# Kernel tuning notes

Hardware: AMD Instinct MI355X
Metric: run time of the kernel (lower is better)

## Reference

```python
import jax, jax.numpy as jnp
import numpy as np

B, H, W, D = 16, 14, 14, 512   # map_dim D == attention_dim A (required by broadcast add)
L, HID, A = 32, 512, 512


def setup_inputs() -> dict:
    key = jax.random.key(0)
    ks = jax.random.split(key, 8)
    s = 0.02
    return {
        "maps": jax.random.normal(ks[0], (B, H, W, D), jnp.float32),
        "hiddens": jax.random.normal(ks[1], (B, L, HID), jnp.float32),
        "W_hidden": jax.random.normal(ks[2], (A, HID), jnp.float32) * s,
        "b_hidden": jnp.zeros((A,), jnp.float32),
        "W_rect": jax.random.normal(ks[3], (1, A), jnp.float32) * s,
        "b_rect": jnp.zeros((1,), jnp.float32),
        "W_co": jax.random.normal(ks[4], (HID, D), jnp.float32) * s,
        "b_co": jnp.zeros((HID,), jnp.float32),
    }


def reference(maps, hiddens, W_hidden, b_hidden, W_rect, b_rect, W_co, b_co):
    b, h, w, d = maps.shape
    fmaps = maps.reshape(b, h * w, d)                       # (B, P, D)
    hlin = hiddens @ W_hidden.T + b_hidden                  # (B, L, A)
    # additive co-attention score: ReLU(fmaps + hlin) -> linear to scalar
    rect = jax.nn.relu(fmaps[:, None, :, :] + hlin[:, :, None, :])  # (B, L, P, A)
    scores = jnp.einsum('blpa,a->blp', rect, W_rect[0]) + b_rect[0]  # (B, L, P)
    attn = jax.nn.softmax(scores, axis=2)                   # softmax over pixels P
    ctx = jnp.einsum('blp,bpd->bld', attn, fmaps)           # (B, L, D)
    co_att = (ctx @ W_co.T + b_co) * hiddens                # (B, L, HID)
    return co_att, attn
```

## Files before the change

kernel.cpp:

```cpp
#include <hip/hip_runtime.h>
#include <math.h>


typedef __attribute__((ext_vector_type(8))) short short8;
typedef __attribute__((ext_vector_type(4))) float f32x4;

__device__ __forceinline__ unsigned f2bf_u(float x) {
    union { float f; unsigned u; } c; c.f = x;
    return (c.u + 0x7FFFu + ((c.u >> 16) & 1u)) >> 16;
}
__device__ __forceinline__ unsigned pack2(float lo, float hi) {
    return f2bf_u(lo) | (f2bf_u(hi) << 16);
}
__device__ __forceinline__ uint4 pack8(const float4 a, const float4 b) {
    uint4 r;
    r.x = pack2(a.x, a.y); r.y = pack2(a.z, a.w);
    r.z = pack2(b.x, b.y); r.w = pack2(b.z, b.w);
    return r;
}

template<int HMUL>
__global__ __launch_bounds__(256) void gemm_kernel(
    const float* __restrict__ Af, const float* __restrict__ Bf,
    const float* __restrict__ bias, const float* __restrict__ hmul,
    float* __restrict__ C)
{
    __shared__ __align__(16) char smem[65536];
    uint4* As = (uint4*)smem;
    uint4* Bs = (uint4*)(smem + 32768);
    float* red = (float*)smem;
    const int tid = threadIdx.x, bid = blockIdx.x;

    const int m0 = (bid >> 4) * 32, n0 = (bid & 15) * 32;
    #pragma unroll
    for (int j = 0; j < 8; ++j) {
        const int S = tid + 256 * j;
        const int i = S >> 6, ln = S & 63;
        const int t = i & 1, s = i >> 1;
        const int row  = t * 16 + (ln & 15);
        const int col8 = s * 4 + (ln >> 4);
        const float* ap = Af + (size_t)(m0 + row) * 512 + col8 * 8;
        const float* bp = Bf + (size_t)(n0 + row) * 512 + col8 * 8;
        As[S] = pack8(*(const float4*)ap, *(const float4*)(ap + 4));
        Bs[S] = pack8(*(const float4*)bp, *(const float4*)(bp + 4));
    }
    __syncthreads();

    const int w = tid >> 6, ln = tid & 63;
    f32x4 acc[4];
    #pragma unroll
    for (int fo = 0; fo < 4; ++fo) acc[fo] = (f32x4){0.f,0.f,0.f,0.f};
    #pragma unroll
    for (int sl = 0; sl < 4; ++sl) {
        const int s = 4 * w + sl;
        const short8 a0 = *(const short8*)&As[(2*s+0)*64 + ln];
        const short8 a1 = *(const short8*)&As[(2*s+1)*64 + ln];
        const short8 b0 = *(const short8*)&Bs[(2*s+0)*64 + ln];
        const short8 b1 = *(const short8*)&Bs[(2*s+1)*64 + ln];
        acc[0] = __builtin_amdgcn_mfma_f32_16x16x32_bf16(a0, b0, acc[0], 0, 0, 0);
        acc[1] = __builtin_amdgcn_mfma_f32_16x16x32_bf16(a0, b1, acc[1], 0, 0, 0);
        acc[2] = __builtin_amdgcn_mfma_f32_16x16x32_bf16(a1, b0, acc[2], 0, 0, 0);
        acc[3] = __builtin_amdgcn_mfma_f32_16x16x32_bf16(a1, b1, acc[3], 0, 0, 0);
    }
    __syncthreads();
    #pragma unroll
    for (int fo = 0; fo < 4; ++fo)
        #pragma unroll
        for (int r = 0; r < 4; ++r)
            red[w*1024 + fo*256 + r*64 + ln] = acc[fo][r];
    __syncthreads();
    #pragma unroll
    for (int j = 0; j < 4; ++j) {
        const int o = tid + 256 * j;
        float v = red[o] + red[1024 + o] + red[2048 + o] + red[3072 + o];
        const int fo = o >> 8, r = (o >> 6) & 3, l2 = o & 63;
        const int m = m0 + (fo >> 1) * 16 + ((l2 >> 4) << 2) + r;
        const int n = n0 + (fo & 1) * 16 + (l2 & 15);
        v += bias[n];
        if (HMUL) v *= hmul[(size_t)m * 512 + n];
        C[(size_t)m * 512 + n] = v;
    }
}

__global__ __launch_bounds__(256) void mid_kernel(
    const float* __restrict__ maps, const float* __restrict__ hlin,
    const float* __restrict__ W_rect, const float* __restrict__ b_rect,
    float* __restrict__ attn_out, float* __restrict__ ctx_out)
{
    const int b = blockIdx.x >> 4, s = blockIdx.x & 15;
    const int l0 = 2 * s;
    const int tid = threadIdx.x;
    const int pi = tid >> 4, k = tid & 15;

    __shared__ float h0[512], h1[512], wv[512];
    __shared__ float ftile[16 * 516];
    __shared__ float red0[208 * 16], red1[208 * 16];
    __shared__ float sm[2 * 208];

    {
        const float4* H0 = (const float4*)(hlin + ((size_t)b * 32 + l0) * 512);
        const float4* H1 = (const float4*)(hlin + ((size_t)b * 32 + l0 + 1) * 512);
        const float4* WV = (const float4*)W_rect;
        if (tid < 128) { ((float4*)h0)[tid] = H0[tid]; ((float4*)wv)[tid] = WV[tid]; }
        else           { ((float4*)h1)[tid - 128] = H1[tid - 128]; }
    }
    __syncthreads();

    int aoff[8];
    float4 h0r[8], h1r[8], wr[8];
    #pragma unroll
    for (int j = 0; j < 8; ++j) {
        aoff[j] = k * 32 + ((j + k) & 7) * 4;
        h0r[j] = *(const float4*)&h0[aoff[j]];
        h1r[j] = *(const float4*)&h1[aoff[j]];
        wr[j]  = *(const float4*)&wv[aoff[j]];
    }

    const float* mb = maps + (size_t)b * 196 * 512;

    for (int c = 0; c < 13; ++c) {
        __syncthreads();
        #pragma unroll
        for (int it = 0; it < 8; ++it) {
            const int idx = tid + 256 * it;
            const int r = idx >> 7, c4 = idx & 127;
            int p = c * 16 + r; if (p > 195) p = 195;
            *(float4*)&ftile[r * 516 + c4 * 4] = *(const float4*)(mb + (size_t)p * 512 + c4 * 4);
        }
        __syncthreads();
        float s0 = 0.f, s1 = 0.f;
        #pragma unroll
        for (int j = 0; j < 8; ++j) {
            const float4 f = *(const float4*)&ftile[pi * 516 + aoff[j]];
            const float4 A = h0r[j], Bv = h1r[j], W = wr[j];
            s0 += fmaxf(f.x + A.x, 0.f) * W.x + fmaxf(f.y + A.y, 0.f) * W.y
                + fmaxf(f.z + A.z, 0.f) * W.z + fmaxf(f.w + A.w, 0.f) * W.w;
            s1 += fmaxf(f.x + Bv.x, 0.f) * W.x + fmaxf(f.y + Bv.y, 0.f) * W.y
                + fmaxf(f.z + Bv.z, 0.f) * W.z + fmaxf(f.w + Bv.w, 0.f) * W.w;
        }
        const int p = c * 16 + pi;
        red0[p * 16 + k] = s0;
        red1[p * 16 + k] = s1;
    }
    __syncthreads();

    const float br = b_rect[0];
    for (int idx = tid; idx < 392; idx += 256) {
        const int l = idx & 1, p = idx >> 1;
        const float* rb = (l ? red1 : red0) + p * 16;
        const float4 a = *(const float4*)rb,      bq = *(const float4*)(rb + 4);
        const float4 cq = *(const float4*)(rb + 8), dq = *(const float4*)(rb + 12);
        sm[l * 208 + p] = (a.x + a.y + a.z + a.w) + (bq.x + bq.y + bq.z + bq.w)
                        + (cq.x + cq.y + cq.z + cq.w) + (dq.x + dq.y + dq.z + dq.w) + br;
    }
    __syncthreads();

    const int wave = tid >> 6, lane = tid & 63;
    if (wave < 2) {
        float v[4];
        #pragma unroll
        for (int i = 0; i < 4; ++i) {
            const int p = lane + 64 * i;
            v[i] = (p < 196) ? sm[wave * 208 + p] : -INFINITY;
        }
        float m = fmaxf(fmaxf(v[0], v[1]), fmaxf(v[2], v[3]));
        for (int off = 32; off > 0; off >>= 1) m = fmaxf(m, __shfl_down(m, off));
        m = __shfl(m, 0);
        float e[4], ssum = 0.f;
        #pragma unroll
        for (int i = 0; i < 4; ++i) {
            const int p = lane + 64 * i;
            e[i] = (p < 196) ? __expf(v[i] - m) : 0.f;
            ssum += e[i];
        }
        for (int off = 32; off > 0; off >>= 1) ssum += __shfl_down(ssum, off);
        ssum = __shfl(ssum, 0);
        const float inv = 1.f / ssum;
        float* ao = attn_out + ((size_t)b * 32 + l0 + wave) * 196;
        #pragma unroll
        for (int i = 0; i < 4; ++i) {
            const int p = lane + 64 * i;
            if (p < 196) {
                const float at = e[i] * inv;
                sm[wave * 208 + p] = at;
                ao[p] = at;
            }
        }
    }
    __syncthreads();

    const int d0 = tid * 2;
    float a0 = 0.f, a1 = 0.f, c0 = 0.f, c1 = 0.f;
    for (int p = 0; p < 196; ++p) {
        const float2 f = *(const float2*)(mb + (size_t)p * 512 + d0);
        const float w0 = sm[p], w1 = sm[208 + p];
        a0 += w0 * f.x; a1 += w0 * f.y;
        c0 += w1 * f.x; c1 += w1 * f.y;
    }
    float2 o0; o0.x = a0; o0.y = a1;
    float2 o1; o1.x = c0; o1.y = c1;
    *(float2*)(ctx_out + ((size_t)b * 32 + l0) * 512 + d0)     = o0;
    *(float2*)(ctx_out + ((size_t)b * 32 + l0 + 1) * 512 + d0) = o1;
}

extern "C" void kernel_launch(void* const* d_in, const int* in_sizes, int n_in,
                              void* d_out, int out_size, void* d_ws, size_t ws_size,
                              hipStream_t stream)
{
    const float* maps     = (const float*)d_in[0];
    const float* hiddens  = (const float*)d_in[1];
    const float* W_hidden = (const float*)d_in[2];
    const float* b_hidden = (const float*)d_in[3];
    const float* W_rect   = (const float*)d_in[4];
    const float* b_rect   = (const float*)d_in[5];
    const float* W_co     = (const float*)d_in[6];
    const float* b_co     = (const float*)d_in[7];

    float* out_co   = (float*)d_out;
    float* out_attn = out_co + (size_t)512 * 512;
    float* ctx      = (float*)d_ws;

    hipLaunchKernelGGL((gemm_kernel<0>), dim3(256), dim3(256), 0, stream,
                       hiddens, W_hidden, b_hidden, (const float*)nullptr, out_co);
    hipLaunchKernelGGL(mid_kernel, dim3(256), dim3(256), 0, stream,
                       maps, out_co, W_rect, b_rect, out_attn, ctx);
    hipLaunchKernelGGL((gemm_kernel<1>), dim3(256), dim3(256), 0, stream,
                       ctx, W_co, b_co, hiddens, out_co);
}
```

Before: 104.5 us.

## Fuse three kernels into one cooperative kernel with grid-wide syncs

Merges the two GEMM kernels and the attention mid kernel into a single cooperative launch. The stages are separated by grid.sync() and share one dynamically partitioned shared-memory buffer. This removes two kernel launch boundaries and the inter-kernel gaps. hlin now goes to a separate workspace instead of out_co. In exchange the whole grid must be co-resident, and the larger shared-memory footprint (about 66 KB) limits occupancy to roughly one block per CU.

```diff
diff --git a/kernel.cpp b/kernel.cpp
--- a/kernel.cpp
+++ b/kernel.cpp
@@ -1,5 +1,8 @@
 #include <hip/hip_runtime.h>
+#include <hip/hip_cooperative_groups.h>
 #include <math.h>
+
+namespace cg = cooperative_groups;
 
 
 typedef __attribute__((ext_vector_type(8))) short short8;
@@ -19,13 +22,14 @@
     return r;
 }
 
+#define SMEM_BYTES 67456
+
 template<int HMUL>
-__global__ __launch_bounds__(256) void gemm_kernel(
+__device__ void gemm_body(char* smem,
     const float* __restrict__ Af, const float* __restrict__ Bf,
     const float* __restrict__ bias, const float* __restrict__ hmul,
     float* __restrict__ C)
 {
-    __shared__ __align__(16) char smem[65536];
     uint4* As = (uint4*)smem;
     uint4* Bs = (uint4*)(smem + 32768);
     float* red = (float*)smem;
@@ -82,7 +86,7 @@
     }
 }
 
-__global__ __launch_bounds__(256) void mid_kernel(
+__device__ void mid_body(char* smem,
     const float* __restrict__ maps, const float* __restrict__ hlin,
     const float* __restrict__ W_rect, const float* __restrict__ b_rect,
     float* __restrict__ attn_out, float* __restrict__ ctx_out)
@@ -92,10 +96,13 @@
     const int tid = threadIdx.x;
     const int pi = tid >> 4, k = tid & 15;
 
-    __shared__ float h0[512], h1[512], wv[512];
-    __shared__ float ftile[16 * 516];
-    __shared__ float red0[208 * 16], red1[208 * 16];
-    __shared__ float sm[2 * 208];
+    float* h0    = (float*)smem;
+    float* h1    = h0 + 512;
+    float* wv    = h1 + 512;
+    float* ftile = wv + 512;
+    float* red0  = ftile + 16 * 516;
+    float* red1  = red0 + 208 * 16;
+    float* smrow = red1 + 208 * 16;
 
     {
         const float4* H0 = (const float4*)(hlin + ((size_t)b * 32 + l0) * 512);
@@ -150,8 +157,8 @@
         const float* rb = (l ? red1 : red0) + p * 16;
         const float4 a = *(const float4*)rb,      bq = *(const float4*)(rb + 4);
         const float4 cq = *(const float4*)(rb + 8), dq = *(const float4*)(rb + 12);
-        sm[l * 208 + p] = (a.x + a.y + a.z + a.w) + (bq.x + bq.y + bq.z + bq.w)
-                        + (cq.x + cq.y + cq.z + cq.w) + (dq.x + dq.y + dq.z + dq.w) + br;
+        smrow[l * 208 + p] = (a.x + a.y + a.z + a.w) + (bq.x + bq.y + bq.z + bq.w)
+                           + (cq.x + cq.y + cq.z + cq.w) + (dq.x + dq.y + dq.z + dq.w) + br;
     }
     __syncthreads();
 
@@ -161,7 +168,7 @@
         #pragma unroll
         for (int i = 0; i < 4; ++i) {
             const int p = lane + 64 * i;
-            v[i] = (p < 196) ? sm[wave * 208 + p] : -INFINITY;
+            v[i] = (p < 196) ? smrow[wave * 208 + p] : -INFINITY;
         }
         float m = fmaxf(fmaxf(v[0], v[1]), fmaxf(v[2], v[3]));
         for (int off = 32; off > 0; off >>= 1) m = fmaxf(m, __shfl_down(m, off));
@@ -182,7 +189,7 @@
             const int p = lane + 64 * i;
             if (p < 196) {
                 const float at = e[i] * inv;
-                sm[wave * 208 + p] = at;
+                smrow[wave * 208 + p] = at;
                 ao[p] = at;
             }
         }
@@ -193,7 +200,7 @@
     float a0 = 0.f, a1 = 0.f, c0 = 0.f, c1 = 0.f;
     for (int p = 0; p < 196; ++p) {
         const float2 f = *(const float2*)(mb + (size_t)p * 512 + d0);
-        const float w0 = sm[p], w1 = sm[208 + p];
+        const float w0 = smrow[p], w1 = smrow[208 + p];
         a0 += w0 * f.x; a1 += w0 * f.y;
         c0 += w1 * f.x; c1 += w1 * f.y;
     }
@@ -201,6 +208,24 @@
     float2 o1; o1.x = c0; o1.y = c1;
     *(float2*)(ctx_out + ((size_t)b * 32 + l0) * 512 + d0)     = o0;
     *(float2*)(ctx_out + ((size_t)b * 32 + l0 + 1) * 512 + d0) = o1;
+}
+
+__global__ __launch_bounds__(256) void fused_kernel(
+    const float* __restrict__ maps, const float* __restrict__ hiddens,
+    const float* __restrict__ W_hidden, const float* __restrict__ b_hidden,
+    const float* __restrict__ W_rect, const float* __restrict__ b_rect,
+    const float* __restrict__ W_co, const float* __restrict__ b_co,
+    float* __restrict__ out_co, float* __restrict__ attn_out,
+    float* __restrict__ hlin_ws, float* __restrict__ ctx_ws)
+{
+    __shared__ __align__(16) char smem[SMEM_BYTES];
+    cg::grid_group grid = cg::this_grid();
+
+    gemm_body<0>(smem, hiddens, W_hidden, b_hidden, (const float*)nullptr, hlin_ws);
+    grid.sync();
+    mid_body(smem, maps, hlin_ws, W_rect, b_rect, attn_out, ctx_ws);
+    grid.sync();
+    gemm_body<1>(smem, ctx_ws, W_co, b_co, hiddens, out_co);
 }
 
 extern "C" void kernel_launch(void* const* d_in, const int* in_sizes, int n_in,
@@ -218,12 +243,14 @@
 
     float* out_co   = (float*)d_out;
     float* out_attn = out_co + (size_t)512 * 512;
-    float* ctx      = (float*)d_ws;
-
-    hipLaunchKernelGGL((gemm_kernel<0>), dim3(256), dim3(256), 0, stream,
-                       hiddens, W_hidden, b_hidden, (const float*)nullptr, out_co);
-    hipLaunchKernelGGL(mid_kernel, dim3(256), dim3(256), 0, stream,
-                       maps, out_co, W_rect, b_rect, out_attn, ctx);
-    hipLaunchKernelGGL((gemm_kernel<1>), dim3(256), dim3(256), 0, stream,
-                       ctx, W_co, b_co, hiddens, out_co);
-}
+    float* hlin     = (float*)d_ws;
+    float* ctx      = hlin + (size_t)512 * 512;
+
+    void* kargs[12] = {
+        (void*)&maps, (void*)&hiddens, (void*)&W_hidden, (void*)&b_hidden,
+        (void*)&W_rect, (void*)&b_rect, (void*)&W_co, (void*)&b_co,
+        (void*)&out_co, (void*)&out_attn, (void*)&hlin, (void*)&ctx
+    };
+    hipLaunchCooperativeKernel((void*)fused_kernel, dim3(256), dim3(256),
+                               kargs, 0, stream);
+}
```

Result: slower. 176.9 us (+69.3%).

## Fuse both projection GEMMs into single co-attention kernel with XCD-aware block mapping

Applied to the files above, without the earlier changes.

Replaces the three-kernel pipeline (bf16 MFMA GEMM, attention middle kernel, second GEMM) with one kernel per (batch, pair of queries) block. That block computes its two hidden projections with fp32 dot products, then scores, softmax and context, and finally applies the W_co projection and the hiddens multiply in place. This removes two launches and the global round trips for hlin and ctx. It also maps blocks so that each XCD handles two batches, aiming for L2 reuse of the maps. In exchange, every block rereads the full W_hidden and W_co matrices (1 MB each) from cache with fp32 CUDA-core math, so the GEMM work is no longer shared across blocks.

```diff
diff --git a/kernel.cpp b/kernel.cpp
--- a/kernel.cpp
+++ b/kernel.cpp
@@ -2,109 +2,63 @@
 #include <math.h>
 
 
-typedef __attribute__((ext_vector_type(8))) short short8;
-typedef __attribute__((ext_vector_type(4))) float f32x4;
-
-__device__ __forceinline__ unsigned f2bf_u(float x) {
-    union { float f; unsigned u; } c; c.f = x;
-    return (c.u + 0x7FFFu + ((c.u >> 16) & 1u)) >> 16;
-}
-__device__ __forceinline__ unsigned pack2(float lo, float hi) {
-    return f2bf_u(lo) | (f2bf_u(hi) << 16);
-}
-__device__ __forceinline__ uint4 pack8(const float4 a, const float4 b) {
-    uint4 r;
-    r.x = pack2(a.x, a.y); r.y = pack2(a.z, a.w);
-    r.z = pack2(b.x, b.y); r.w = pack2(b.z, b.w);
-    return r;
-}
-
-template<int HMUL>
-__global__ __launch_bounds__(256) void gemm_kernel(
-    const float* __restrict__ Af, const float* __restrict__ Bf,
-    const float* __restrict__ bias, const float* __restrict__ hmul,
-    float* __restrict__ C)
+__global__ __launch_bounds__(256) void coatt_kernel(
+    const float* __restrict__ maps, const float* __restrict__ hiddens,
+    const float* __restrict__ W_hidden, const float* __restrict__ b_hidden,
+    const float* __restrict__ W_rect, const float* __restrict__ b_rect,
+    const float* __restrict__ W_co, const float* __restrict__ b_co,
+    float* __restrict__ out_co, float* __restrict__ attn_out)
 {
-    __shared__ __align__(16) char smem[65536];
-    uint4* As = (uint4*)smem;
-    uint4* Bs = (uint4*)(smem + 32768);
-    float* red = (float*)smem;
-    const int tid = threadIdx.x, bid = blockIdx.x;
-
-    const int m0 = (bid >> 4) * 32, n0 = (bid & 15) * 32;
-    #pragma unroll
-    for (int j = 0; j < 8; ++j) {
-        const int S = tid + 256 * j;
-        const int i = S >> 6, ln = S & 63;
-        const int t = i & 1, s = i >> 1;
-        const int row  = t * 16 + (ln & 15);
-        const int col8 = s * 4 + (ln >> 4);
-        const float* ap = Af + (size_t)(m0 + row) * 512 + col8 * 8;
-        const float* bp = Bf + (size_t)(n0 + row) * 512 + col8 * 8;
-        As[S] = pack8(*(const float4*)ap, *(const float4*)(ap + 4));
-        Bs[S] = pack8(*(const float4*)bp, *(const float4*)(bp + 4));
-    }
-    __syncthreads();
-
-    const int w = tid >> 6, ln = tid & 63;
-    f32x4 acc[4];
-    #pragma unroll
-    for (int fo = 0; fo < 4; ++fo) acc[fo] = (f32x4){0.f,0.f,0.f,0.f};
-    #pragma unroll
-    for (int sl = 0; sl < 4; ++sl) {
-        const int s = 4 * w + sl;
-        const short8 a0 = *(const short8*)&As[(2*s+0)*64 + ln];
-        const short8 a1 = *(const short8*)&As[(2*s+1)*64 + ln];
-        const short8 b0 = *(const short8*)&Bs[(2*s+0)*64 + ln];
-        const short8 b1 = *(const short8*)&Bs[(2*s+1)*64 + ln];
-        acc[0] = __builtin_amdgcn_mfma_f32_16x16x32_bf16(a0, b0, acc[0], 0, 0, 0);
-        acc[1] = __builtin_amdgcn_mfma_f32_16x16x32_bf16(a0, b1, acc[1], 0, 0, 0);
-        acc[2] = __builtin_amdgcn_mfma_f32_16x16x32_bf16(a1, b0, acc[2], 0, 0, 0);
-        acc[3] = __builtin_amdgcn_mfma_f32_16x16x32_bf16(a1, b1, acc[3], 0, 0, 0);
-    }
-    __syncthreads();
-    #pragma unroll
-    for (int fo = 0; fo < 4; ++fo)
-        #pragma unroll
-        for (int r = 0; r < 4; ++r)
-            red[w*1024 + fo*256 + r*64 + ln] = acc[fo][r];
-    __syncthreads();
-    #pragma unroll
-    for (int j = 0; j < 4; ++j) {
-        const int o = tid + 256 * j;
-        float v = red[o] + red[1024 + o] + red[2048 + o] + red[3072 + o];
-        const int fo = o >> 8, r = (o >> 6) & 3, l2 = o & 63;
-        const int m = m0 + (fo >> 1) * 16 + ((l2 >> 4) << 2) + r;
-        const int n = n0 + (fo & 1) * 16 + (l2 & 15);
-        v += bias[n];
-        if (HMUL) v *= hmul[(size_t)m * 512 + n];
-        C[(size_t)m * 512 + n] = v;
-    }
-}
-
-__global__ __launch_bounds__(256) void mid_kernel(
-    const float* __restrict__ maps, const float* __restrict__ hlin,
-    const float* __restrict__ W_rect, const float* __restrict__ b_rect,
-    float* __restrict__ attn_out, float* __restrict__ ctx_out)
-{
-    const int b = blockIdx.x >> 4, s = blockIdx.x & 15;
-    const int l0 = 2 * s;
-    const int tid = threadIdx.x;
+    __shared__ __align__(16) float arena[17888];
+    float* hidA  = arena;
+    float* hidB  = arena + 512;
+    float* wv    = arena + 1024;
+    float* h0    = arena + 1536;
+    float* h1    = arena + 2048;
+    float* ftile = arena + 2560;
+    float* red0  = arena + 10816;
+    float* red1  = arena + 14144;
+    float* smrow = arena + 17472;
+    float* ctx0  = red0;
+    float* ctx1  = red0 + 512;
+
+    const int tid = threadIdx.x, bx = blockIdx.x;
+    const int xcd = bx & 7, idx = bx >> 3;
+    const int b  = (xcd << 1) | (idx & 1);
+    const int l0 = (idx >> 1) * 2;
+
+    {
+        const float4* HA = (const float4*)(hiddens + ((size_t)b * 32 + l0) * 512);
+        const float4* HB = (const float4*)(hiddens + ((size_t)b * 32 + l0 + 1) * 512);
+        const float4* WV = (const float4*)W_rect;
+        if (tid < 128) { ((float4*)hidA)[tid] = HA[tid]; ((float4*)wv)[tid] = WV[tid]; }
+        else           { ((float4*)hidB)[tid - 128] = HB[tid - 128]; }
+    }
+    __syncthreads();
+
+    {
+        const int n0 = tid, n1 = tid + 256;
+        const float4* wr0 = (const float4*)(W_hidden + (size_t)n0 * 512);
+        const float4* wr1 = (const float4*)(W_hidden + (size_t)n1 * 512);
+        const float4* a4 = (const float4*)hidA;
+        const float4* b4 = (const float4*)hidB;
+        float s00 = 0.f, s01 = 0.f, s10 = 0.f, s11 = 0.f;
+        #pragma unroll 8
+        for (int j = 0; j < 128; ++j) {
+            const float4 w0 = wr0[j], w1 = wr1[j];
+            const float4 ha = a4[j], hb = b4[j];
+            s00 += w0.x*ha.x + w0.y*ha.y + w0.z*ha.z + w0.w*ha.w;
+            s01 += w0.x*hb.x + w0.y*hb.y + w0.z*hb.z + w0.w*hb.w;
+            s10 += w1.x*ha.x + w1.y*ha.y + w1.z*ha.z + w1.w*ha.w;
+            s11 += w1.x*hb.x + w1.y*hb.y + w1.z*hb.z + w1.w*hb.w;
+        }
+        const float bi0 = b_hidden[n0], bi1 = b_hidden[n1];
+        h0[n0] = s00 + bi0;  h1[n0] = s01 + bi0;
+        h0[n1] = s10 + bi1;  h1[n1] = s11 + bi1;
+    }
+    __syncthreads();
+
     const int pi = tid >> 4, k = tid & 15;
-
-    __shared__ float h0[512], h1[512], wv[512];
-    __shared__ float ftile[16 * 516];
-    __shared__ float red0[208 * 16], red1[208 * 16];
-    __shared__ float sm[2 * 208];
-
-    {
-        const float4* H0 = (const float4*)(hlin + ((size_t)b * 32 + l0) * 512);
-        const float4* H1 = (const float4*)(hlin + ((size_t)b * 32 + l0 + 1) * 512);
-        const float4* WV = (const float4*)W_rect;
-        if (tid < 128) { ((float4*)h0)[tid] = H0[tid]; ((float4*)wv)[tid] = WV[tid]; }
-        else           { ((float4*)h1)[tid - 128] = H1[tid - 128]; }
-    }
-    __syncthreads();
 
     int aoff[8];
     float4 h0r[8], h1r[8], wr[8];
@@ -122,8 +76,8 @@
         __syncthreads();
         #pragma unroll
         for (int it = 0; it < 8; ++it) {
-            const int idx = tid + 256 * it;
-            const int r = idx >> 7, c4 = idx & 127;
+            const int idx2 = tid + 256 * it;
+            const int r = idx2 >> 7, c4 = idx2 & 127;
             int p = c * 16 + r; if (p > 195) p = 195;
             *(float4*)&ftile[r * 516 + c4 * 4] = *(const float4*)(mb + (size_t)p * 512 + c4 * 4);
         }
@@ -145,13 +99,13 @@
     __syncthreads();
 
     const float br = b_rect[0];
-    for (int idx = tid; idx < 392; idx += 256) {
-        const int l = idx & 1, p = idx >> 1;
+    for (int i2 = tid; i2 < 392; i2 += 256) {
+        const int l = i2 & 1, p = i2 >> 1;
         const float* rb = (l ? red1 : red0) + p * 16;
         const float4 a = *(const float4*)rb,      bq = *(const float4*)(rb + 4);
         const float4 cq = *(const float4*)(rb + 8), dq = *(const float4*)(rb + 12);
-        sm[l * 208 + p] = (a.x + a.y + a.z + a.w) + (bq.x + bq.y + bq.z + bq.w)
-                        + (cq.x + cq.y + cq.z + cq.w) + (dq.x + dq.y + dq.z + dq.w) + br;
+        smrow[l * 208 + p] = (a.x + a.y + a.z + a.w) + (bq.x + bq.y + bq.z + bq.w)
+                           + (cq.x + cq.y + cq.z + cq.w) + (dq.x + dq.y + dq.z + dq.w) + br;
     }
     __syncthreads();
 
@@ -161,7 +115,7 @@
         #pragma unroll
         for (int i = 0; i < 4; ++i) {
             const int p = lane + 64 * i;
-            v[i] = (p < 196) ? sm[wave * 208 + p] : -INFINITY;
+            v[i] = (p < 196) ? smrow[wave * 208 + p] : -INFINITY;
         }
         float m = fmaxf(fmaxf(v[0], v[1]), fmaxf(v[2], v[3]));
         for (int off = 32; off > 0; off >>= 1) m = fmaxf(m, __shfl_down(m, off));
@@ -182,25 +136,54 @@
             const int p = lane + 64 * i;
             if (p < 196) {
                 const float at = e[i] * inv;
-                sm[wave * 208 + p] = at;
+                smrow[wave * 208 + p] = at;
                 ao[p] = at;
             }
         }
     }
     __syncthreads();
 
-    const int d0 = tid * 2;
-    float a0 = 0.f, a1 = 0.f, c0 = 0.f, c1 = 0.f;
-    for (int p = 0; p < 196; ++p) {
-        const float2 f = *(const float2*)(mb + (size_t)p * 512 + d0);
-        const float w0 = sm[p], w1 = sm[208 + p];
-        a0 += w0 * f.x; a1 += w0 * f.y;
-        c0 += w1 * f.x; c1 += w1 * f.y;
-    }
-    float2 o0; o0.x = a0; o0.y = a1;
-    float2 o1; o1.x = c0; o1.y = c1;
-    *(float2*)(ctx_out + ((size_t)b * 32 + l0) * 512 + d0)     = o0;
-    *(float2*)(ctx_out + ((size_t)b * 32 + l0 + 1) * 512 + d0) = o1;
+    {
+        const int d0 = tid * 2;
+        float a0 = 0.f, a1 = 0.f, c0 = 0.f, c1 = 0.f;
+        for (int p = 0; p < 196; ++p) {
+            const float2 f = *(const float2*)(mb + (size_t)p * 512 + d0);
+            const float w0 = smrow[p], w1 = smrow[208 + p];
+            a0 += w0 * f.x; a1 += w0 * f.y;
+            c0 += w1 * f.x; c1 += w1 * f.y;
+        }
+        __syncthreads();
+        float2 o0; o0.x = a0; o0.y = a1;
+        float2 o1; o1.x = c0; o1.y = c1;
+        *(float2*)&ctx0[d0] = o0;
+        *(float2*)&ctx1[d0] = o1;
+    }
+    __syncthreads();
+
+    {
+        const int n0 = tid, n1 = tid + 256;
+        const float4* wr0 = (const float4*)(W_co + (size_t)n0 * 512);
+        const float4* wr1 = (const float4*)(W_co + (size_t)n1 * 512);
+        const float4* c04 = (const float4*)ctx0;
+        const float4* c14 = (const float4*)ctx1;
+        float s00 = 0.f, s01 = 0.f, s10 = 0.f, s11 = 0.f;
+        #pragma unroll 8
+        for (int j = 0; j < 128; ++j) {
+            const float4 w0 = wr0[j], w1 = wr1[j];
+            const float4 ca = c04[j], cb = c14[j];
+            s00 += w0.x*ca.x + w0.y*ca.y + w0.z*ca.z + w0.w*ca.w;
+            s01 += w0.x*cb.x + w0.y*cb.y + w0.z*cb.z + w0.w*cb.w;
+            s10 += w1.x*ca.x + w1.y*ca.y + w1.z*ca.z + w1.w*ca.w;
+            s11 += w1.x*cb.x + w1.y*cb.y + w1.z*cb.z + w1.w*cb.w;
+        }
+        const float bc0 = b_co[n0], bc1 = b_co[n1];
+        float* o0 = out_co + ((size_t)b * 32 + l0) * 512;
+        float* o1 = out_co + ((size_t)b * 32 + l0 + 1) * 512;
+        o0[n0] = (s00 + bc0) * hidA[n0];
+        o1[n0] = (s01 + bc0) * hidB[n0];
+        o0[n1] = (s10 + bc1) * hidA[n1];
+        o1[n1] = (s11 + bc1) * hidB[n1];
+    }
 }
 
 extern "C" void kernel_launch(void* const* d_in, const int* in_sizes, int n_in,
@@ -218,12 +201,8 @@
 
     float* out_co   = (float*)d_out;
     float* out_attn = out_co + (size_t)512 * 512;
-    float* ctx      = (float*)d_ws;
-
-    hipLaunchKernelGGL((gemm_kernel<0>), dim3(256), dim3(256), 0, stream,
-                       hiddens, W_hidden, b_hidden, (const float*)nullptr, out_co);
-    hipLaunchKernelGGL(mid_kernel, dim3(256), dim3(256), 0, stream,
-                       maps, out_co, W_rect, b_rect, out_attn, ctx);
-    hipLaunchKernelGGL((gemm_kernel<1>), dim3(256), dim3(256), 0, stream,
-                       ctx, W_co, b_co, hiddens, out_co);
+
+    hipLaunchKernelGGL(coatt_kernel, dim3(256), dim3(256), 0, stream,
+                       maps, hiddens, W_hidden, b_hidden, W_rect, b_rect,
+                       W_co, b_co, out_co, out_attn);
 }
```

Measured after the change: 151.1 us. +44.6%, slower.

## Fuse three kernels into one persistent kernel with grid barriers

Applied to the files above, without the earlier changes.

Merges the hidden projection GEMM, the attention/softmax/context stage and the output GEMM into one 256-block, 512-thread kernel separated by software grid barriers built on a global atomic counter. The intent is to remove two kernel launch gaps. The mid stage is also rewritten: each wave computes per-pixel scores straight from global memory using wave shuffles instead of staging an LDS tile. Blocks are mapped so that batches stay together per XCD. Risks are the cost of the spin barrier, a possible deadlock if not all 256 blocks are co-resident, and the counter never being reset between calls.

```diff
diff --git a/kernel.cpp b/kernel.cpp
--- a/kernel.cpp
+++ b/kernel.cpp
@@ -4,6 +4,23 @@
 
 typedef __attribute__((ext_vector_type(8))) short short8;
 typedef __attribute__((ext_vector_type(4))) float f32x4;
+
+__device__ unsigned g_bar = 0;
+
+__device__ __forceinline__ void grid_barrier() {
+    __syncthreads();
+    if (threadIdx.x == 0) {
+        __threadfence();
+        unsigned old = __hip_atomic_fetch_add(&g_bar, 1u, __ATOMIC_ACQ_REL,
+                                              __HIP_MEMORY_SCOPE_AGENT);
+        const unsigned tgt = (old & ~255u) + 256u;
+        while (__hip_atomic_load(&g_bar, __ATOMIC_ACQUIRE,
+                                 __HIP_MEMORY_SCOPE_AGENT) < tgt)
+            __builtin_amdgcn_s_sleep(2);
+        __threadfence();
+    }
+    __syncthreads();
+}
 
 __device__ __forceinline__ unsigned f2bf_u(float x) {
     union { float f; unsigned u; } c; c.f = x;
@@ -18,14 +35,22 @@
     r.z = pack2(b.x, b.y); r.w = pack2(b.z, b.w);
     return r;
 }
+__device__ __forceinline__ float rdot4(const float4 f, const float4 g, const float4 w) {
+    return fmaxf(f.x+g.x, 0.f)*w.x + fmaxf(f.y+g.y, 0.f)*w.y
+         + fmaxf(f.z+g.z, 0.f)*w.z + fmaxf(f.w+g.w, 0.f)*w.w;
+}
+__device__ __forceinline__ float wave_sum(float v) {
+    v += __shfl_down(v, 32); v += __shfl_down(v, 16); v += __shfl_down(v, 8);
+    v += __shfl_down(v, 4);  v += __shfl_down(v, 2);  v += __shfl_down(v, 1);
+    return v;
+}
 
 template<int HMUL>
-__global__ __launch_bounds__(256) void gemm_kernel(
+__device__ __forceinline__ void gemm_body(char* smem,
     const float* __restrict__ Af, const float* __restrict__ Bf,
     const float* __restrict__ bias, const float* __restrict__ hmul,
     float* __restrict__ C)
 {
-    __shared__ __align__(16) char smem[65536];
     uint4* As = (uint4*)smem;
     uint4* Bs = (uint4*)(smem + 32768);
     float* red = (float*)smem;
@@ -33,8 +58,8 @@
 
     const int m0 = (bid >> 4) * 32, n0 = (bid & 15) * 32;
     #pragma unroll
-    for (int j = 0; j < 8; ++j) {
-        const int S = tid + 256 * j;
+    for (int j = 0; j < 4; ++j) {
+        const int S = tid + 512 * j;
         const int i = S >> 6, ln = S & 63;
         const int t = i & 1, s = i >> 1;
         const int row  = t * 16 + (ln & 15);
@@ -51,8 +76,8 @@
     #pragma unroll
     for (int fo = 0; fo < 4; ++fo) acc[fo] = (f32x4){0.f,0.f,0.f,0.f};
     #pragma unroll
-    for (int sl = 0; sl < 4; ++sl) {
-        const int s = 4 * w + sl;
+    for (int sl = 0; sl < 2; ++sl) {
+        const int s = 2 * w + sl;
         const short8 a0 = *(const short8*)&As[(2*s+0)*64 + ln];
         const short8 a1 = *(const short8*)&As[(2*s+1)*64 + ln];
         const short8 b0 = *(const short8*)&Bs[(2*s+0)*64 + ln];
@@ -70,9 +95,11 @@
             red[w*1024 + fo*256 + r*64 + ln] = acc[fo][r];
     __syncthreads();
     #pragma unroll
-    for (int j = 0; j < 4; ++j) {
-        const int o = tid + 256 * j;
-        float v = red[o] + red[1024 + o] + red[2048 + o] + red[3072 + o];
+    for (int jj = 0; jj < 2; ++jj) {
+        const int o = tid + 512 * jj;
+        float v = 0.f;
+        #pragma unroll
+        for (int ww = 0; ww < 8; ++ww) v += red[ww*1024 + o];
         const int fo = o >> 8, r = (o >> 6) & 3, l2 = o & 63;
         const int m = m0 + (fo >> 1) * 16 + ((l2 >> 4) << 2) + r;
         const int n = n0 + (fo & 1) * 16 + (l2 & 15);
@@ -82,86 +109,59 @@
     }
 }
 
-__global__ __launch_bounds__(256) void mid_kernel(
+__device__ __forceinline__ void mid_body(float* smrow,
     const float* __restrict__ maps, const float* __restrict__ hlin,
     const float* __restrict__ W_rect, const float* __restrict__ b_rect,
     float* __restrict__ attn_out, float* __restrict__ ctx_out)
 {
-    const int b = blockIdx.x >> 4, s = blockIdx.x & 15;
-    const int l0 = 2 * s;
-    const int tid = threadIdx.x;
-    const int pi = tid >> 4, k = tid & 15;
-
-    __shared__ float h0[512], h1[512], wv[512];
-    __shared__ float ftile[16 * 516];
-    __shared__ float red0[208 * 16], red1[208 * 16];
-    __shared__ float sm[2 * 208];
-
-    {
-        const float4* H0 = (const float4*)(hlin + ((size_t)b * 32 + l0) * 512);
-        const float4* H1 = (const float4*)(hlin + ((size_t)b * 32 + l0 + 1) * 512);
-        const float4* WV = (const float4*)W_rect;
-        if (tid < 128) { ((float4*)h0)[tid] = H0[tid]; ((float4*)wv)[tid] = WV[tid]; }
-        else           { ((float4*)h1)[tid - 128] = H1[tid - 128]; }
-    }
-    __syncthreads();
-
-    int aoff[8];
-    float4 h0r[8], h1r[8], wr[8];
-    #pragma unroll
-    for (int j = 0; j < 8; ++j) {
-        aoff[j] = k * 32 + ((j + k) & 7) * 4;
-        h0r[j] = *(const float4*)&h0[aoff[j]];
-        h1r[j] = *(const float4*)&h1[aoff[j]];
-        wr[j]  = *(const float4*)&wv[aoff[j]];
-    }
-
+    const int tid = threadIdx.x, bx = blockIdx.x;
+    const int xcd = bx & 7, idx = bx >> 3;
+    const int b  = (xcd << 1) | (idx & 1);
+    const int l0 = (idx >> 1) * 2;
+    const int w = tid >> 6, lane = tid & 63;
+    const int a_lo = lane * 4, a_hi = 256 + lane * 4;
+
+    const float* h0p = hlin + ((size_t)b * 32 + l0) * 512;
+    const float* h1p = h0p + 512;
+    const float4 g0_lo = *(const float4*)(h0p + a_lo);
+    const float4 g0_hi = *(const float4*)(h0p + a_hi);
+    const float4 g1_lo = *(const float4*)(h1p + a_lo);
+    const float4 g1_hi = *(const float4*)(h1p + a_hi);
+    const float4 w_lo  = *(const float4*)(W_rect + a_lo);
+    const float4 w_hi  = *(const float4*)(W_rect + a_hi);
+    const float br = b_rect[0];
     const float* mb = maps + (size_t)b * 196 * 512;
 
-    for (int c = 0; c < 13; ++c) {
-        __syncthreads();
-        #pragma unroll
-        for (int it = 0; it < 8; ++it) {
-            const int idx = tid + 256 * it;
-            const int r = idx >> 7, c4 = idx & 127;
-            int p = c * 16 + r; if (p > 195) p = 195;
-            *(float4*)&ftile[r * 516 + c4 * 4] = *(const float4*)(mb + (size_t)p * 512 + c4 * 4);
-        }
-        __syncthreads();
-        float s0 = 0.f, s1 = 0.f;
-        #pragma unroll
-        for (int j = 0; j < 8; ++j) {
-            const float4 f = *(const float4*)&ftile[pi * 516 + aoff[j]];
-            const float4 A = h0r[j], Bv = h1r[j], W = wr[j];
-            s0 += fmaxf(f.x + A.x, 0.f) * W.x + fmaxf(f.y + A.y, 0.f) * W.y
-                + fmaxf(f.z + A.z, 0.f) * W.z + fmaxf(f.w + A.w, 0.f) * W.w;
-            s1 += fmaxf(f.x + Bv.x, 0.f) * W.x + fmaxf(f.y + Bv.y, 0.f) * W.y
-                + fmaxf(f.z + Bv.z, 0.f) * W.z + fmaxf(f.w + Bv.w, 0.f) * W.w;
-        }
-        const int p = c * 16 + pi;
-        red0[p * 16 + k] = s0;
-        red1[p * 16 + k] = s1;
-    }
-    __syncthreads();
-
-    const float br = b_rect[0];
-    for (int idx = tid; idx < 392; idx += 256) {
-        const int l = idx & 1, p = idx >> 1;
-        const float* rb = (l ? red1 : red0) + p * 16;
-        const float4 a = *(const float4*)rb,      bq = *(const float4*)(rb + 4);
-        const float4 cq = *(const float4*)(rb + 8), dq = *(const float4*)(rb + 12);
-        sm[l * 208 + p] = (a.x + a.y + a.z + a.w) + (bq.x + bq.y + bq.z + bq.w)
-                        + (cq.x + cq.y + cq.z + cq.w) + (dq.x + dq.y + dq.z + dq.w) + br;
-    }
-    __syncthreads();
-
-    const int wave = tid >> 6, lane = tid & 63;
-    if (wave < 2) {
+    for (int p0 = w; p0 < 196; p0 += 16) {
+        const int p1 = p0 + 8;
+        const float* fr0 = mb + (size_t)p0 * 512;
+        const float4 fa0 = *(const float4*)(fr0 + a_lo);
+        const float4 fb0 = *(const float4*)(fr0 + a_hi);
+        float s00 = rdot4(fa0, g0_lo, w_lo) + rdot4(fb0, g0_hi, w_hi);
+        float s01 = rdot4(fa0, g1_lo, w_lo) + rdot4(fb0, g1_hi, w_hi);
+        float s10 = 0.f, s11 = 0.f;
+        if (p1 < 196) {
+            const float* fr1 = mb + (size_t)p1 * 512;
+            const float4 fa1 = *(const float4*)(fr1 + a_lo);
+            const float4 fb1 = *(const float4*)(fr1 + a_hi);
+            s10 = rdot4(fa1, g0_lo, w_lo) + rdot4(fb1, g0_hi, w_hi);
+            s11 = rdot4(fa1, g1_lo, w_lo) + rdot4(fb1, g1_hi, w_hi);
+        }
+        s00 = wave_sum(s00); s01 = wave_sum(s01);
+        s10 = wave_sum(s10); s11 = wave_sum(s11);
+        if (lane == 0) {
+            smrow[p0] = s00 + br; smrow[208 + p0] = s01 + br;
+            if (p1 < 196) { smrow[p1] = s10 + br; smrow[208 + p1] = s11 + br; }
+        }
+    }
+    __syncthreads();
+
+    if (w < 2) {
         float v[4];
         #pragma unroll
         for (int i = 0; i < 4; ++i) {
             const int p = lane + 64 * i;
-            v[i] = (p < 196) ? sm[wave * 208 + p] : -INFINITY;
+            v[i] = (p < 196) ? smrow[w * 208 + p] : -INFINITY;
         }
         float m = fmaxf(fmaxf(v[0], v[1]), fmaxf(v[2], v[3]));
         for (int off = 32; off > 0; off >>= 1) m = fmaxf(m, __shfl_down(m, off));
@@ -176,31 +176,54 @@
         for (int off = 32; off > 0; off >>= 1) ssum += __shfl_down(ssum, off);
         ssum = __shfl(ssum, 0);
         const float inv = 1.f / ssum;
-        float* ao = attn_out + ((size_t)b * 32 + l0 + wave) * 196;
+        float* ao = attn_out + ((size_t)b * 32 + l0 + w) * 196;
         #pragma unroll
         for (int i = 0; i < 4; ++i) {
             const int p = lane + 64 * i;
             if (p < 196) {
                 const float at = e[i] * inv;
-                sm[wave * 208 + p] = at;
+                smrow[w * 208 + p] = at;
                 ao[p] = at;
             }
         }
     }
     __syncthreads();
 
-    const int d0 = tid * 2;
-    float a0 = 0.f, a1 = 0.f, c0 = 0.f, c1 = 0.f;
-    for (int p = 0; p < 196; ++p) {
-        const float2 f = *(const float2*)(mb + (size_t)p * 512 + d0);
-        const float w0 = sm[p], w1 = sm[208 + p];
-        a0 += w0 * f.x; a1 += w0 * f.y;
-        c0 += w1 * f.x; c1 += w1 * f.y;
-    }
-    float2 o0; o0.x = a0; o0.y = a1;
-    float2 o1; o1.x = c0; o1.y = c1;
-    *(float2*)(ctx_out + ((size_t)b * 32 + l0) * 512 + d0)     = o0;
-    *(float2*)(ctx_out + ((size_t)b * 32 + l0 + 1) * 512 + d0) = o1;
+    {
+        const int d = tid;
+        float a0=0.f,a1=0.f,a2=0.f,a3=0.f, c0=0.f,c1=0.f,c2=0.f,c3=0.f;
+        for (int p = 0; p < 196; p += 4) {
+            const float f0 = mb[(size_t)(p+0)*512 + d];
+            const float f1 = mb[(size_t)(p+1)*512 + d];
+            const float f2 = mb[(size_t)(p+2)*512 + d];
+            const float f3 = mb[(size_t)(p+3)*512 + d];
+            a0 += smrow[p+0]*f0; a1 += smrow[p+1]*f1;
+            a2 += smrow[p+2]*f2; a3 += smrow[p+3]*f3;
+            c0 += smrow[208+p+0]*f0; c1 += smrow[208+p+1]*f1;
+            c2 += smrow[208+p+2]*f2; c3 += smrow[208+p+3]*f3;
+        }
+        float* cx = ctx_out + ((size_t)b * 32 + l0) * 512;
+        cx[d]       = (a0 + a1) + (a2 + a3);
+        cx[512 + d] = (c0 + c1) + (c2 + c3);
+    }
+}
+
+__global__ __launch_bounds__(512) void coatt_fused(
+    const float* __restrict__ maps, const float* __restrict__ hiddens,
+    const float* __restrict__ W_hidden, const float* __restrict__ b_hidden,
+    const float* __restrict__ W_rect, const float* __restrict__ b_rect,
+    const float* __restrict__ W_co, const float* __restrict__ b_co,
+    float* __restrict__ out_co, float* __restrict__ attn_out,
+    float* __restrict__ hlin_ws, float* __restrict__ ctx_ws)
+{
+    __shared__ __align__(16) char smem[65536];
+    __shared__ __align__(16) float smrow[2 * 208];
+
+    gemm_body<0>(smem, hiddens, W_hidden, b_hidden, (const float*)nullptr, hlin_ws);
+    grid_barrier();
+    mid_body(smrow, maps, hlin_ws, W_rect, b_rect, attn_out, ctx_ws);
+    grid_barrier();
+    gemm_body<1>(smem, ctx_ws, W_co, b_co, hiddens, out_co);
 }
 
 extern "C" void kernel_launch(void* const* d_in, const int* in_sizes, int n_in,
@@ -218,12 +241,10 @@
 
     float* out_co   = (float*)d_out;
     float* out_attn = out_co + (size_t)512 * 512;
-    float* ctx      = (float*)d_ws;
-
-    hipLaunchKernelGGL((gemm_kernel<0>), dim3(256), dim3(256), 0, stream,
-                       hiddens, W_hidden, b_hidden, (const float*)nullptr, out_co);
-    hipLaunchKernelGGL(mid_kernel, dim3(256), dim3(256), 0, stream,
-                       maps, out_co, W_rect, b_rect, out_attn, ctx);
-    hipLaunchKernelGGL((gemm_kernel<1>), dim3(256), dim3(256), 0, stream,
-                       ctx, W_co, b_co, hiddens, out_co);
-}
+    float* hlin     = (float*)d_ws;
+    float* ctx      = hlin + (size_t)512 * 512;
+
+    hipLaunchKernelGGL(coatt_fused, dim3(256), dim3(512), 0, stream,
+                       maps, hiddens, W_hidden, b_hidden, W_rect, b_rect,
+                       W_co, b_co, out_co, out_attn, hlin, ctx);
+}
```

After: 148.3 us. +41.9%, slower.
